# Performance work log

Measured on AMD Instinct MI355X. Metric: run time of the kernel, lower is better.

## Reference

```python
import jax, jax.numpy as jnp
import numpy as np

BS, N, D = 8, 2048, 512


def setup_inputs() -> dict:
    key = jax.random.key(0)
    ks = jax.random.split(key, 8)
    s = 0.05  # small scale keeps exp(k + bias) numerically tame
    inp = jax.random.normal(ks[0], (BS, N, D), dtype=jnp.float32)
    Wq = jax.random.normal(ks[1], (D, D), dtype=jnp.float32) * s
    bq = jax.random.normal(ks[2], (D,), dtype=jnp.float32) * s
    Wk = jax.random.normal(ks[3], (D, D), dtype=jnp.float32) * s
    bk = jax.random.normal(ks[4], (D,), dtype=jnp.float32) * s
    Wv = jax.random.normal(ks[5], (D, D), dtype=jnp.float32) * s
    bv = jax.random.normal(ks[6], (D,), dtype=jnp.float32) * s
    pos_bias = jax.random.normal(ks[7], (N, N), dtype=jnp.float32) * s
    return {"input": inp, "Wq": Wq, "bq": bq, "Wk": Wk, "bk": bk,
            "Wv": Wv, "bv": bv, "pos_bias": pos_bias}


def reference(input, Wq, bq, Wk, bk, Wv, bv, pos_bias):
    # q, k, v projections: (bs, n, d)
    q = input @ Wq + bq
    k = input @ Wk + bk
    v = input @ Wv + bv
    # AFT-Full: out[b,i,d] = sigmoid(q)[b,i,d] *
    #   sum_j exp(k[b,j,d] + B[i,j]) * v[b,j,d] / sum_j exp(k[b,j,d] + B[i,j])
    # Factor exp(k + B) = exp(B) * exp(k): avoids the (n,bs,n,d) broadcast,
    # identical math to the torch source.
    ek = jnp.exp(k)                       # (bs, n, d)
    eB = jnp.exp(pos_bias)                # (n, n), rows = query pos i
    numerator = jnp.einsum('ij,bjd->bid', eB, ek * v)
    denominator = jnp.einsum('ij,bjd->bid', eB, ek)
    return jax.nn.sigmoid(q) * (numerator / denominator)
```

## Files before the change

### kernel.cpp

```cpp
#include <hip/hip_runtime.h>
#include <stdint.h>

#define N_SEQ 2048
#define D_MODEL 512
#define MROWS 16384
#define NT_K 32

typedef __attribute__((ext_vector_type(8))) short bf16x8;
typedef __attribute__((ext_vector_type(4))) float f32x4;

__device__ __forceinline__ short f2bf(float f) {
  union { float f; uint32_t u; } x; x.f = f;
  uint32_t r = x.u + 0x7FFFu + ((x.u >> 16) & 1u);
  return (short)(uint16_t)(r >> 16);
}
__device__ __forceinline__ unsigned short f2h(float f) {
  union { _Float16 h; unsigned short u; } x; x.h = (_Float16)f; return x.u;
}
__device__ __forceinline__ float h2f(unsigned short u) {
  union { unsigned short u; _Float16 h; } x; x.u = u; return (float)x.h;
}

__device__ __forceinline__ void gload_lds16(const void* g, void* l) {
  __builtin_amdgcn_global_load_lds(
      (__attribute__((address_space(1))) void*)(void*)g,
      (__attribute__((address_space(3))) void*)l, 16, 0, 0);
}


__global__ void k_conv_bf16(const float* __restrict__ in,
                            short* __restrict__ a, int n4) {
  int stride = gridDim.x * blockDim.x;
  for (int i = blockIdx.x * blockDim.x + threadIdx.x; i < n4; i += stride) {
    float4 v = reinterpret_cast<const float4*>(in)[i];
    short4 h;
    h.x = f2bf(v.x); h.y = f2bf(v.y); h.z = f2bf(v.z); h.w = f2bf(v.w);
    reinterpret_cast<short4*>(a)[i] = h;
  }
}

__global__ void k_prep_eb(const float* __restrict__ pb, short* __restrict__ eb,
                          int n4) {
  int stride = gridDim.x * blockDim.x;
  for (int i = blockIdx.x * blockDim.x + threadIdx.x; i < n4; i += stride) {
    float4 v = reinterpret_cast<const float4*>(pb)[i];
    short4 o;
    o.x = f2bf(expf(v.x));
    o.y = f2bf(expf(v.y));
    o.z = f2bf(expf(v.z));
    o.w = f2bf(expf(v.w));
    reinterpret_cast<short4*>(eb)[i] = o;
  }
}

__global__ void k_prep_w(const float* __restrict__ Wq, const float* __restrict__ Wk,
                         const float* __restrict__ Wv, short* __restrict__ wh) {
  int t = blockIdx.x * blockDim.x + threadIdx.x;
  if (t >= 1536 * 512) return;
  int c = t >> 9, k = t & 511;
  float v;
  if (c < 512) v = Wq[k * 512 + c];
  else {
    int cc = c - 512, d = cc >> 1;
    v = (cc & 1) ? Wv[k * 512 + d] : Wk[k * 512 + d];
  }
  wh[t] = f2bf(v);
}

__global__ __launch_bounds__(256) void k_proj(
    const short* __restrict__ A, const short* __restrict__ W,
    const float* __restrict__ bq, const float* __restrict__ bk,
    const float* __restrict__ bv,
    unsigned short* __restrict__ sigq, short* __restrict__ Xf) {
  __shared__ short lA[128 * 64], lB[128 * 64];
  const int tid = threadIdx.x;
  const int lane = tid & 63, wid = tid >> 6;
  const int wr = wid >> 1, wc = wid & 1;
  const int lrow = lane & 15;
  const int kq = (lane >> 4) << 4;
  const int row0 = blockIdx.x * 128;
  const int col0 = blockIdx.y * 128;

  const f32x4 fzero = {0.f, 0.f, 0.f, 0.f};
  f32x4 acc[4][4];
#pragma unroll
  for (int m = 0; m < 4; ++m)
#pragma unroll
    for (int n = 0; n < 4; ++n) acc[m][n] = fzero;

  const short* gA = A + row0 * 512;
  const short* gB = W + col0 * 512;

  for (int kt = 0; kt < 8; ++kt) {
    const int kb = kt * 64;
#pragma unroll
    for (int p = 0; p < 4; ++p) {
      int c = p * 256 + tid;
      int B = c << 4;
      int r = B >> 7;
      int wp = (B & 127) ^ ((r & 7) << 4);
      int ke = wp >> 1;
      int goff = r * 512 + kb + ke;
      int loff = (p * 256 + wid * 64) << 3;
      gload_lds16(gA + goff, lA + loff);
      gload_lds16(gB + goff, lB + loff);
    }
    __syncthreads();
#pragma unroll
    for (int ks = 0; ks < 2; ++ks) {
      int kb2 = kq + ks * 64;
      bf16x8 fb[4];
#pragma unroll
      for (int n = 0; n < 4; ++n) {
        int r = wc * 64 + n * 16 + lrow;
        fb[n] = *(const bf16x8*)((const char*)lB + (r << 7) +
                                 (kb2 ^ ((r & 7) << 4)));
      }
#pragma unroll
      for (int m = 0; m < 4; ++m) {
        int r = wr * 64 + m * 16 + lrow;
        bf16x8 fa = *(const bf16x8*)((const char*)lA + (r << 7) +
                                     (kb2 ^ ((r & 7) << 4)));
#pragma unroll
        for (int n = 0; n < 4; ++n)
          acc[m][n] = __builtin_amdgcn_mfma_f32_16x16x32_bf16(fa, fb[n], acc[m][n], 0, 0, 0);
      }
    }
    __syncthreads();
  }

  const int rbase = row0 + wr * 64 + ((lane >> 4) << 2);
  if (col0 < 512) {
#pragma unroll
    for (int n = 0; n < 4; ++n) {
      int c = col0 + wc * 64 + n * 16 + lrow;
      float bias = bq[c];
#pragma unroll
      for (int m = 0; m < 4; ++m) {
        int gr = rbase + m * 16;
#pragma unroll
        for (int r = 0; r < 4; ++r) {
          float q = acc[m][n][r] + bias;
          sigq[(gr + r) * 512 + c] = f2h(1.f / (1.f + expf(-q)));
        }
      }
    }
  } else {
    int s = lane & 1;
#pragma unroll
    for (int n = 0; n < 4; ++n) {
      int c = col0 + wc * 64 + n * 16 + lrow;
      int d = (c - 512) >> 1;
      float bias = s ? bv[d] : bk[d];
#pragma unroll
      for (int m = 0; m < 4; ++m) {
        int gr = rbase + m * 16;
        int b = gr >> 11;
        int j = gr & 2047;
        f32x4 val;
#pragma unroll
        for (int r = 0; r < 4; ++r) val[r] = acc[m][n][r] + bias;
        if (!s) {
#pragma unroll
          for (int r = 0; r < 4; ++r) val[r] = expf(val[r]);
        }
        f32x4 oth;
#pragma unroll
        for (int r = 0; r < 4; ++r) oth[r] = __shfl_xor(val[r], 1);
        if (!s) {
          short4 wq, eq;
          wq.x = f2bf(val[0] * oth[0]); eq.x = f2bf(val[0]);
          wq.y = f2bf(val[1] * oth[1]); eq.y = f2bf(val[1]);
          wq.z = f2bf(val[2] * oth[2]); eq.z = f2bf(val[2]);
          wq.w = f2bf(val[3] * oth[3]); eq.w = f2bf(val[3]);
          int colp = b * 1024 + 2 * d;
          int kg = j >> 5;
          int sub = ((j >> 3) & 3) << 4;
          int e0 = j & 4;
          int ctn = colp >> 4;
          int lnn = (colp & 15) | sub;
          int lnd = ((colp + 1) & 15) | sub;
          *(short4*)&Xf[(((ctn * 64 + kg) * 64 + lnn) << 3) + e0] = wq;
          *(short4*)&Xf[(((ctn * 64 + kg) * 64 + lnd) << 3) + e0] = eq;
        }
      }
    }
  }
}

__global__ __launch_bounds__(1024, 4) void k_main3(
    const short* __restrict__ eB, const short* __restrict__ Xf,
    const unsigned short* __restrict__ sigq, float* __restrict__ out) {
  extern __shared__ short lds[];
  const int tid = threadIdx.x;
  const int lane = tid & 63, wid = tid >> 6;
  const int wr = wid >> 2, wc = wid & 3;
  const int lrow = lane & 15;
  const int khi = (lane >> 4) << 4;

  const int bid = blockIdx.x;
  const int xcd = bid & 7, bj = bid >> 3;
  const int row0 = (bj & 7) * 256;
  const int col0 = ((xcd << 2) + (bj >> 3)) * 256;

  const f32x4 fzero = {0.f, 0.f, 0.f, 0.f};
  f32x4 acc[4][4];
#pragma unroll
  for (int m = 0; m < 4; ++m)
#pragma unroll
    for (int n = 0; n < 4; ++n) acc[m][n] = fzero;

  const short* gA = eB + row0 * 2048;
  const int ctbase = (col0 >> 4) + wc * 4;

  auto STAGE = [&](int kt) {
    const short* src = gA + kt * 64;
    const int sb = (kt & 1) << 14;
#pragma unroll
    for (int p = 0; p < 2; ++p) {
      int c = p * 1024 + tid;
      int r = c >> 3;
      int ke = ((((c & 7) << 4) ^ ((r & 7) << 4)) >> 1);
      gload_lds16(src + r * 2048 + ke,
                  lds + sb + ((p * 1024 + wid * 64) << 3));
    }
  };
  auto LDA = [&](int b, int ks, int m) -> bf16x8 {
    int R = wr * 64 + m * 16 + lrow;
    int kb = ks * 64 + khi;
    return *(const bf16x8*)((const char*)lds + (b << 15) + R * 128 +
                            (kb ^ ((R & 7) << 4)));
  };
  auto LDBg = [&](int kt, int ks, int n) -> bf16x8 {
    int ct = ctbase + n;
    int kg = kt * 2 + ks;
    return *(const bf16x8*)(Xf + ((((ct << 6) + kg) << 6) + lane) * 8);
  };

  STAGE(0);
  __syncthreads();

  for (int t = 0; t < NT_K; ++t) {
    const int b = t & 1;
    if (t + 1 < NT_K) STAGE(t + 1);
#pragma unroll
    for (int ks = 0; ks < 2; ++ks) {
      bf16x8 fb[4], fa[4];
#pragma unroll
      for (int n = 0; n < 4; ++n) fb[n] = LDBg(t, ks, n);
#pragma unroll
      for (int m = 0; m < 4; ++m) fa[m] = LDA(b, ks, m);
#pragma unroll
      for (int m = 0; m < 4; ++m)
#pragma unroll
        for (int n = 0; n < 4; ++n)
          acc[m][n] = __builtin_amdgcn_mfma_f32_16x16x32_bf16(fa[m], fb[n], acc[m][n], 0, 0, 0);
    }
    __syncthreads();
  }

  const int rbase = row0 + wr * 64 + ((lane >> 4) << 2);
#pragma unroll
  for (int n = 0; n < 4; ++n) {
    int c = col0 + wc * 64 + n * 16 + lrow;
    int b = c >> 10;
    int d = (c & 1023) >> 1;
#pragma unroll
    for (int m = 0; m < 4; ++m) {
      f32x4 den;
#pragma unroll
      for (int r = 0; r < 4; ++r) den[r] = __shfl_xor(acc[m][n][r], 1);
      if ((lane & 1) == 0) {
#pragma unroll
        for (int r = 0; r < 4; ++r) {
          int i2 = rbase + m * 16 + r;
          int idx = (b * 2048 + i2) * 512 + d;
          out[idx] = h2f(sigq[idx]) * (acc[m][n][r] / den[r]);
        }
      }
    }
  }
}

extern "C" void kernel_launch(void* const* d_in, const int* in_sizes, int n_in,
                              void* d_out, int out_size, void* d_ws, size_t ws_size,
                              hipStream_t stream) {
  const float* in = (const float*)d_in[0];
  const float* Wq = (const float*)d_in[1];
  const float* bq = (const float*)d_in[2];
  const float* Wk = (const float*)d_in[3];
  const float* bk = (const float*)d_in[4];
  const float* Wv = (const float*)d_in[5];
  const float* bv = (const float*)d_in[6];
  const float* pb = (const float*)d_in[7];
  float* out = (float*)d_out;

  char* ws = (char*)d_ws;
  short* Xf = (short*)ws;
  short* eB = (short*)(ws + 33554432);
  short* Ah = (short*)(ws + 41943040);
  short* Wh = (short*)(ws + 58720256);
  unsigned short* sigq = (unsigned short*)(ws + 60293120);

  (void)hipFuncSetAttribute((const void*)k_main3,
                            hipFuncAttributeMaxDynamicSharedMemorySize, 65536);

  k_conv_bf16<<<2048, 256, 0, stream>>>(in, Ah, MROWS * D_MODEL / 4);
  k_prep_w<<<3072, 256, 0, stream>>>(Wq, Wk, Wv, Wh);
  k_prep_eb<<<2048, 256, 0, stream>>>(pb, eB, N_SEQ * N_SEQ / 4);

  dim3 gp(128, 12);
  k_proj<<<gp, 256, 0, stream>>>(Ah, Wh, bq, bk, bv, sigq, Xf);

  k_main3<<<dim3(256), 1024, 65536, stream>>>(eB, Xf, sigq, out);
}
```

Before: 150.2 us.

## Halve main GEMM block tile width and prefetch B fragments from global

The main eB×X GEMM kernel now uses 512-thread blocks covering 256x128 output tiles, launched as 512 blocks instead of 256, with 8 waves arranged 4x2. B-operand fragments read directly from global memory are now software-prefetched one k-substep ahead into registers, so global load latency overlaps the MFMA work. Each tile re-stages the same eB rows from global into LDS twice as often, and the extra prefetch buffer adds register pressure.

```diff
diff --git a/kernel.cpp b/kernel.cpp
--- a/kernel.cpp
+++ b/kernel.cpp
@@ -188,20 +188,20 @@
   }
 }
 
-__global__ __launch_bounds__(1024, 4) void k_main3(
+__global__ __launch_bounds__(512, 4) void k_main5(
     const short* __restrict__ eB, const short* __restrict__ Xf,
     const unsigned short* __restrict__ sigq, float* __restrict__ out) {
   extern __shared__ short lds[];
   const int tid = threadIdx.x;
   const int lane = tid & 63, wid = tid >> 6;
-  const int wr = wid >> 2, wc = wid & 3;
+  const int wr = wid >> 1, wc = wid & 1;
   const int lrow = lane & 15;
   const int khi = (lane >> 4) << 4;
 
   const int bid = blockIdx.x;
   const int xcd = bid & 7, bj = bid >> 3;
   const int row0 = (bj & 7) * 256;
-  const int col0 = ((xcd << 2) + (bj >> 3)) * 256;
+  const int col0 = ((xcd << 3) + (bj >> 3)) * 128;
 
   const f32x4 fzero = {0.f, 0.f, 0.f, 0.f};
   f32x4 acc[4][4];
@@ -217,12 +217,12 @@
     const short* src = gA + kt * 64;
     const int sb = (kt & 1) << 14;
 #pragma unroll
-    for (int p = 0; p < 2; ++p) {
-      int c = p * 1024 + tid;
+    for (int p = 0; p < 4; ++p) {
+      int c = p * 512 + tid;
       int r = c >> 3;
       int ke = ((((c & 7) << 4) ^ ((r & 7) << 4)) >> 1);
       gload_lds16(src + r * 2048 + ke,
-                  lds + sb + ((p * 1024 + wid * 64) << 3));
+                  lds + sb + ((p * 512 + wid * 64) << 3));
     }
   };
   auto LDA = [&](int b, int ks, int m) -> bf16x8 {
@@ -231,31 +231,49 @@
     return *(const bf16x8*)((const char*)lds + (b << 15) + R * 128 +
                             (kb ^ ((R & 7) << 4)));
   };
-  auto LDBg = [&](int kt, int ks, int n) -> bf16x8 {
-    int ct = ctbase + n;
-    int kg = kt * 2 + ks;
-    return *(const bf16x8*)(Xf + ((((ct << 6) + kg) << 6) + lane) * 8);
+  auto LOADFB = [&](bf16x8* fb, int kt, int ks) {
+#pragma unroll
+    for (int n = 0; n < 4; ++n) {
+      int ct = ctbase + n;
+      int kg = kt * 2 + ks;
+      fb[n] = *(const bf16x8*)(Xf + ((((ct << 6) + kg) << 6) + lane) * 8);
+    }
   };
 
+  bf16x8 fb[8];
+
   STAGE(0);
+  LOADFB(fb, 0, 0);
+  LOADFB(fb + 4, 0, 1);
   __syncthreads();
 
   for (int t = 0; t < NT_K; ++t) {
     const int b = t & 1;
     if (t + 1 < NT_K) STAGE(t + 1);
-#pragma unroll
-    for (int ks = 0; ks < 2; ++ks) {
-      bf16x8 fb[4], fa[4];
-#pragma unroll
-      for (int n = 0; n < 4; ++n) fb[n] = LDBg(t, ks, n);
-#pragma unroll
-      for (int m = 0; m < 4; ++m) fa[m] = LDA(b, ks, m);
+    {
+      bf16x8 fa[4];
+#pragma unroll
+      for (int m = 0; m < 4; ++m) fa[m] = LDA(b, 0, m);
 #pragma unroll
       for (int m = 0; m < 4; ++m)
 #pragma unroll
         for (int n = 0; n < 4; ++n)
-          acc[m][n] = __builtin_amdgcn_mfma_f32_16x16x32_bf16(fa[m], fb[n], acc[m][n], 0, 0, 0);
-    }
+          acc[m][n] = __builtin_amdgcn_mfma_f32_16x16x32_bf16(
+              fa[m], fb[n], acc[m][n], 0, 0, 0);
+    }
+    if (t + 1 < NT_K) LOADFB(fb, t + 1, 0);
+    {
+      bf16x8 fa[4];
+#pragma unroll
+      for (int m = 0; m < 4; ++m) fa[m] = LDA(b, 1, m);
+#pragma unroll
+      for (int m = 0; m < 4; ++m)
+#pragma unroll
+        for (int n = 0; n < 4; ++n)
+          acc[m][n] = __builtin_amdgcn_mfma_f32_16x16x32_bf16(
+              fa[m], fb[4 + n], acc[m][n], 0, 0, 0);
+    }
+    if (t + 1 < NT_K) LOADFB(fb + 4, t + 1, 1);
     __syncthreads();
   }
 
@@ -302,7 +320,7 @@
   short* Wh = (short*)(ws + 58720256);
   unsigned short* sigq = (unsigned short*)(ws + 60293120);
 
-  (void)hipFuncSetAttribute((const void*)k_main3,
+  (void)hipFuncSetAttribute((const void*)k_main5,
                             hipFuncAttributeMaxDynamicSharedMemorySize, 65536);
 
   k_conv_bf16<<<2048, 256, 0, stream>>>(in, Ah, MROWS * D_MODEL / 4);
@@ -312,5 +330,5 @@
   dim3 gp(128, 12);
   k_proj<<<gp, 256, 0, stream>>>(Ah, Wh, bq, bk, bv, sigq, Xf);
 
-  k_main3<<<dim3(256), 1024, 65536, stream>>>(eB, Xf, sigq, out);
-}
+  k_main5<<<dim3(512), 512, 65536, stream>>>(eB, Xf, sigq, out);
+}
```

After: 149.5 us. Within noise of the previous version (-0.5%).

## Retile main GEMM to 256x128 blocks with register-prefetched B and MFMA priority

Applied to the files above, without the earlier changes.

The main eB x Xf GEMM now uses 512-thread blocks on 256x128 output tiles, giving twice as many blocks. The B fragments from global memory are prefetched into registers one k-tile ahead, so their latency overlaps the current MFMAs. A-tile LDS staging uses precomputed swizzled offsets, and s_setprio raises wave priority around the MFMA bursts. The trade is more register pressure from holding eight B fragments, plus more total A-tile traffic, since each A row block is now loaded by twice as many blocks.

```diff
diff --git a/kernel.cpp b/kernel.cpp
--- a/kernel.cpp
+++ b/kernel.cpp
@@ -188,20 +188,65 @@
   }
 }
 
-__global__ __launch_bounds__(1024, 4) void k_main3(
+
+#define MFMA16(A_, B_, C_) __builtin_amdgcn_mfma_f32_16x16x32_bf16(A_, B_, C_, 0, 0, 0)
+
+#define LDA6(BUF, KS, M)                                                     \
+  (*(const bf16x8*)((const char*)lds + ((vbase ^ ((KS) << 6)) + (M) * 2048 + \
+                                        ((BUF) << 15))))
+
+#define LOADFB6(DST, T, KS)                                                  \
+  {                                                                          \
+    _Pragma("unroll") for (int n_ = 0; n_ < 4; ++n_) {                       \
+      (DST)[n_] = *(const bf16x8*)(Xf + (((size_t)(ctu + n_)) << 15) +       \
+                                   ((((T) * 2 + (KS))) << 9) + lvo);         \
+    }                                                                        \
+  }
+
+#define MMH6(BUF, KS, FBH)                                                   \
+  {                                                                          \
+    bf16x8 fa0 = LDA6(BUF, KS, 0), fa1 = LDA6(BUF, KS, 1),                   \
+           fa2 = LDA6(BUF, KS, 2), fa3 = LDA6(BUF, KS, 3);                   \
+    __builtin_amdgcn_s_setprio(1);                                           \
+    _Pragma("unroll") for (int n_ = 0; n_ < 4; ++n_) {                       \
+      acc[0][n_] = MFMA16(fa0, (FBH)[n_], acc[0][n_]);                       \
+      acc[1][n_] = MFMA16(fa1, (FBH)[n_], acc[1][n_]);                       \
+      acc[2][n_] = MFMA16(fa2, (FBH)[n_], acc[2][n_]);                       \
+      acc[3][n_] = MFMA16(fa3, (FBH)[n_], acc[3][n_]);                       \
+    }                                                                        \
+    __builtin_amdgcn_s_setprio(0);                                           \
+  }
+
+#define TILE6(T, BUF)                                                        \
+  {                                                                          \
+    if ((T) + 1 < NT_K) {                                                    \
+      const int tk_ = ((T) + 1) << 6;                                        \
+      gload_lds16(gA + svo0 + tk_, ldst0 + (((BUF) ^ 1) << 14));             \
+      gload_lds16(gA + svo0 + 131072 + tk_, ldst1 + (((BUF) ^ 1) << 14));    \
+      gload_lds16(gA + svo0 + 262144 + tk_, ldst2 + (((BUF) ^ 1) << 14));    \
+      gload_lds16(gA + svo0 + 393216 + tk_, ldst3 + (((BUF) ^ 1) << 14));    \
+    }                                                                        \
+    MMH6(BUF, 0, fb);                                                        \
+    if ((T) + 1 < NT_K) LOADFB6(fb, (T) + 1, 0);                             \
+    MMH6(BUF, 1, fb + 4);                                                    \
+    if ((T) + 1 < NT_K) LOADFB6(fb + 4, (T) + 1, 1);                         \
+    __syncthreads();                                                         \
+  }
+
+__global__ __launch_bounds__(512, 4) void k_main6(
     const short* __restrict__ eB, const short* __restrict__ Xf,
     const unsigned short* __restrict__ sigq, float* __restrict__ out) {
   extern __shared__ short lds[];
   const int tid = threadIdx.x;
   const int lane = tid & 63, wid = tid >> 6;
-  const int wr = wid >> 2, wc = wid & 3;
+  const int wr = wid >> 1, wc = wid & 1;
   const int lrow = lane & 15;
   const int khi = (lane >> 4) << 4;
 
   const int bid = blockIdx.x;
   const int xcd = bid & 7, bj = bid >> 3;
   const int row0 = (bj & 7) * 256;
-  const int col0 = ((xcd << 2) + (bj >> 3)) * 256;
+  const int col0 = ((xcd << 3) + (bj >> 3)) * 128;
 
   const f32x4 fzero = {0.f, 0.f, 0.f, 0.f};
   f32x4 acc[4][4];
@@ -211,52 +256,31 @@
     for (int n = 0; n < 4; ++n) acc[m][n] = fzero;
 
   const short* gA = eB + row0 * 2048;
-  const int ctbase = (col0 >> 4) + wc * 4;
-
-  auto STAGE = [&](int kt) {
-    const short* src = gA + kt * 64;
-    const int sb = (kt & 1) << 14;
-#pragma unroll
-    for (int p = 0; p < 2; ++p) {
-      int c = p * 1024 + tid;
-      int r = c >> 3;
-      int ke = ((((c & 7) << 4) ^ ((r & 7) << 4)) >> 1);
-      gload_lds16(src + r * 2048 + ke,
-                  lds + sb + ((p * 1024 + wid * 64) << 3));
-    }
-  };
-  auto LDA = [&](int b, int ks, int m) -> bf16x8 {
-    int R = wr * 64 + m * 16 + lrow;
-    int kb = ks * 64 + khi;
-    return *(const bf16x8*)((const char*)lds + (b << 15) + R * 128 +
-                            (kb ^ ((R & 7) << 4)));
-  };
-  auto LDBg = [&](int kt, int ks, int n) -> bf16x8 {
-    int ct = ctbase + n;
-    int kg = kt * 2 + ks;
-    return *(const bf16x8*)(Xf + ((((ct << 6) + kg) << 6) + lane) * 8);
-  };
-
-  STAGE(0);
+
+  const int sw = (lrow & 7) << 4;
+  const int vbase = (wr * 64 + lrow) * 128 + (khi ^ sw);
+  const int svo0 = ((tid >> 3) * 2048) +
+                   (((((tid & 7) << 4) ^ (((tid >> 3) & 7) << 4))) >> 1);
+  short* ldst0 = lds + (wid << 9);
+  short* ldst1 = lds + 4096 + (wid << 9);
+  short* ldst2 = lds + 8192 + (wid << 9);
+  short* ldst3 = lds + 12288 + (wid << 9);
+  const int ctu = __builtin_amdgcn_readfirstlane((col0 >> 4) + wc * 4);
+  const int lvo = lane << 3;
+
+  bf16x8 fb[8];
+
+  gload_lds16(gA + svo0, ldst0);
+  gload_lds16(gA + svo0 + 131072, ldst1);
+  gload_lds16(gA + svo0 + 262144, ldst2);
+  gload_lds16(gA + svo0 + 393216, ldst3);
+  LOADFB6(fb, 0, 0);
+  LOADFB6(fb + 4, 0, 1);
   __syncthreads();
 
-  for (int t = 0; t < NT_K; ++t) {
-    const int b = t & 1;
-    if (t + 1 < NT_K) STAGE(t + 1);
-#pragma unroll
-    for (int ks = 0; ks < 2; ++ks) {
-      bf16x8 fb[4], fa[4];
-#pragma unroll
-      for (int n = 0; n < 4; ++n) fb[n] = LDBg(t, ks, n);
-#pragma unroll
-      for (int m = 0; m < 4; ++m) fa[m] = LDA(b, ks, m);
-#pragma unroll
-      for (int m = 0; m < 4; ++m)
-#pragma unroll
-        for (int n = 0; n < 4; ++n)
-          acc[m][n] = __builtin_amdgcn_mfma_f32_16x16x32_bf16(fa[m], fb[n], acc[m][n], 0, 0, 0);
-    }
-    __syncthreads();
+  for (int t = 0; t < NT_K; t += 2) {
+    TILE6(t, 0);
+    TILE6(t + 1, 1);
   }
 
   const int rbase = row0 + wr * 64 + ((lane >> 4) << 2);
@@ -302,7 +326,7 @@
   short* Wh = (short*)(ws + 58720256);
   unsigned short* sigq = (unsigned short*)(ws + 60293120);
 
-  (void)hipFuncSetAttribute((const void*)k_main3,
+  (void)hipFuncSetAttribute((const void*)k_main6,
                             hipFuncAttributeMaxDynamicSharedMemorySize, 65536);
 
   k_conv_bf16<<<2048, 256, 0, stream>>>(in, Ah, MROWS * D_MODEL / 4);
@@ -312,5 +336,5 @@
   dim3 gp(128, 12);
   k_proj<<<gp, 256, 0, stream>>>(Ah, Wh, bq, bk, bv, sigq, Xf);
 
-  k_main3<<<dim3(256), 1024, 65536, stream>>>(eB, Xf, sigq, out);
-}
+  k_main6<<<dim3(512), 512, 65536, stream>>>(eB, Xf, sigq, out);
+}
```

Result: slower. 342.3 us (+127.9%).
